# Kernel tuning notes

Measured on AMD Instinct MI355X. Metric: run time of the kernel, lower is better.

The kernel has to match this reference:

```python
import jax, jax.numpy as jnp
import numpy as np

EPS = 1e-3  # Keras BatchNormalization default epsilon
HEADS = 4
KEY_DEPTH = 16   # k
INTRA = 1        # u
VAL_DEPTH = 64   # v = kernel_out // heads = 256 // 4
C_IN = 256
B, HH, WW = 16, 32, 32
N = HH * WW      # == size of positional embedding


def setup_inputs() -> dict:
    key = jax.random.key(0)
    ks = jax.random.split(key, 6)
    x = jax.random.normal(ks[0], (B, HH, WW, C_IN), dtype=jnp.float32)
    # 1x1 conv kernels == dense matrices over the channel dim
    Wq = jax.random.normal(ks[1], (C_IN, KEY_DEPTH * HEADS), dtype=jnp.float32) * 0.05
    Wk = jax.random.normal(ks[2], (C_IN, KEY_DEPTH * INTRA), dtype=jnp.float32) * 0.05
    Wv = jax.random.normal(ks[3], (C_IN, VAL_DEPTH * INTRA), dtype=jnp.float32) * 0.05
    # BatchNorm (inference mode) parameters
    gamma_q = jnp.ones((KEY_DEPTH * HEADS,), jnp.float32)
    beta_q = jnp.zeros((KEY_DEPTH * HEADS,), jnp.float32)
    mean_q = jnp.zeros((KEY_DEPTH * HEADS,), jnp.float32)
    var_q = jnp.ones((KEY_DEPTH * HEADS,), jnp.float32)
    gamma_v = jnp.ones((VAL_DEPTH * INTRA,), jnp.float32)
    beta_v = jnp.zeros((VAL_DEPTH * INTRA,), jnp.float32)
    mean_v = jnp.zeros((VAL_DEPTH * INTRA,), jnp.float32)
    var_v = jnp.ones((VAL_DEPTH * INTRA,), jnp.float32)
    # Positional embedding: [size, size, key_depth, intra_depth], uniform init
    E = jax.random.uniform(ks[4], (N, N, KEY_DEPTH, INTRA), dtype=jnp.float32)
    return {
        'x': x, 'Wq': Wq, 'Wk': Wk, 'Wv': Wv,
        'gamma_q': gamma_q, 'beta_q': beta_q, 'mean_q': mean_q, 'var_q': var_q,
        'gamma_v': gamma_v, 'beta_v': beta_v, 'mean_v': mean_v, 'var_v': var_v,
        'E': E,
    }


def _bn(t, gamma, beta, mean, var):
    return gamma * (t - mean) / jnp.sqrt(var + EPS) + beta


def reference(x, Wq, Wk, Wv, gamma_q, beta_q, mean_q, var_q,
              gamma_v, beta_v, mean_v, var_v, E):
    b, hh, ww, _ = x.shape
    n = hh * ww
    # 1x1 conv projections (context c == x)
    q = jnp.einsum('bhwc,cd->bhwd', x, Wq)           # [b,hh,ww,h*k]
    k = jnp.einsum('bhwc,cd->bhwd', x, Wk)           # [b,hh,ww,u*k]
    v = jnp.einsum('bhwc,cd->bhwd', x, Wv)           # [b,hh,ww,u*v]
    q = _bn(q, gamma_q, beta_q, mean_q, var_q)
    v = _bn(v, gamma_v, beta_v, mean_v, var_v)
    # softmax over the channel axis (faithful to the source code)
    k = jax.nn.softmax(k, axis=-1)
    # rearranges: b hh ww (h k) -> b h k n ; b hh ww (u k) -> b u k n ; b hh ww (u v) -> b u v n
    q = q.reshape(b, n, HEADS, KEY_DEPTH).transpose(0, 2, 3, 1)   # [b,h,k,n]
    k = k.reshape(b, n, INTRA, KEY_DEPTH).transpose(0, 2, 3, 1)   # [b,u,k,n]
    v = v.reshape(b, n, INTRA, VAL_DEPTH).transpose(0, 2, 3, 1)   # [b,u,v,n]
    # content lambda: sum over intra-depth and positions
    lam_c = jnp.einsum('bukn,buvn->bkv', k, v)                    # [b,k,v]
    Yc = jnp.einsum('bhkn,bkv->bhvn', q, lam_c)                   # [b,h,v,n]
    # positional lambdas: E[n,m,k,u] contracted with v[b,u,v,m]
    lam_p = jnp.einsum('nmku,buvm->bnkv', E, v)                   # [b,n,k,v]
    Yp = jnp.einsum('bhkn,bnkv->bhvn', q, lam_p)                  # [b,h,v,n]
    Y = Yc + Yp                                                    # [b,h,v,n]
    # b h v n -> b hh ww (h v)
    out = Y.transpose(0, 3, 1, 2).reshape(b, hh, ww, HEADS * VAL_DEPTH)
    return out
```

## Files before the change

### kernel.cpp

```cpp
#include <hip/hip_runtime.h>
#include <stdint.h>

#define EPS 1e-3f

typedef __bf16 bf16x8 __attribute__((ext_vector_type(8)));
typedef float  f32x4  __attribute__((ext_vector_type(4)));

static __device__ __forceinline__ uint16_t f2bf(float f) {
  union { __bf16 b; uint16_t u; } r; r.b = (__bf16)f; return r.u;
}
static __device__ __forceinline__ uint32_t cvt2(float lo, float hi) {
  union { __bf16 b[2]; uint32_t u; } r;
  r.b[0] = (__bf16)lo; r.b[1] = (__bf16)hi;
  return r.u;
}
static __device__ __forceinline__ void gload_lds16(const void* g, void* l) {
  __builtin_amdgcn_global_load_lds(
      (const __attribute__((address_space(1))) unsigned int*)g,
      (__attribute__((address_space(3))) unsigned int*)l, 16, 0, 0);
}

__global__ __launch_bounds__(256) void wprep(
    const float* __restrict__ Wq, const float* __restrict__ Wk,
    const float* __restrict__ Wv, uint16_t* __restrict__ WtP)
{
  const int col = blockIdx.x, t = threadIdx.x;
  float val = (col < 64) ? Wq[t * 64 + col]
            : (col < 80) ? Wk[t * 16 + (col - 64)]
                         : Wv[t * 64 + (col - 80)];
  WtP[col * 264 + t] = f2bf(val);
}

__global__ __launch_bounds__(256) void proj_mfma(
    const float* __restrict__ x, const uint16_t* __restrict__ WtP,
    const float* __restrict__ gq, const float* __restrict__ bq,
    const float* __restrict__ mq, const float* __restrict__ vq,
    const float* __restrict__ gv, const float* __restrict__ bv,
    const float* __restrict__ mv, const float* __restrict__ vvp,
    float* __restrict__ Qf, uint16_t* __restrict__ VbfT,
    float* __restrict__ part)
{
  __shared__ __align__(16) char smem[111616];
  uint16_t* const xA = (uint16_t*)smem;
  char* const Wt = smem + 33792;

  const int t = threadIdx.x;
  const int wid = t >> 6, lane = t & 63;
  const int bid = blockIdx.x;
  const int b = bid >> 4, mc = bid & 15;
  const int r0 = b * 1024 + mc * 64;

#pragma unroll
  for (int i = 0; i < 19; ++i) {
    int off = (i * 256 + t) * 16;
    gload_lds16((const char*)WtP + off, Wt + off);
  }
  {
    const int row = t >> 2, ks0 = (t & 3) * 64;
    const float* src = x + (size_t)(r0 + row) * 256 + ks0;
    uint16_t* dstp = xA + row * 264 + ks0;
#pragma unroll
    for (int i = 0; i < 8; ++i) {
      float4 d0 = *(const float4*)(src + i * 8);
      float4 d1 = *(const float4*)(src + i * 8 + 4);
      uint4 q;
      q.x = cvt2(d0.x, d0.y); q.y = cvt2(d0.z, d0.w);
      q.z = cvt2(d1.x, d1.y); q.w = cvt2(d1.z, d1.w);
      *(uint4*)(dstp + i * 8) = q;
    }
  }
  __syncthreads();

  f32x4 acc[9];
#pragma unroll
  for (int f = 0; f < 9; ++f) acc[f] = f32x4{0.f, 0.f, 0.f, 0.f};
  const int arow = wid * 16 + (lane & 15);
#pragma unroll
  for (int kst = 0; kst < 8; ++kst) {
    const int sb = kst * 64 + ((lane >> 4) << 4);
    bf16x8 af = *(const bf16x8*)((const char*)xA + arow * 528 + sb);
#pragma unroll
    for (int f = 0; f < 9; ++f) {
      const int crow = f * 16 + (lane & 15);
      bf16x8 bfr = *(const bf16x8*)(Wt + crow * 528 + sb);
      acc[f] = __builtin_amdgcn_mfma_f32_16x16x32_bf16(af, bfr, acc[f], 0, 0, 0);
    }
  }

  const int cl = lane & 15;
  const int rbase = wid * 16 + ((lane >> 4) << 2);

  float qs[4], qb[4], qm[4], vs[4], vb[4], vm[4];
#pragma unroll
  for (int f = 0; f < 4; ++f) {
    const int c = f * 16 + cl;
    qs[f] = gq[c] * rsqrtf(vq[c] + EPS); qb[f] = bq[c]; qm[f] = mq[c];
    vs[f] = gv[c] * rsqrtf(vvp[c] + EPS); vb[f] = bv[c]; vm[f] = mv[c];
  }
#pragma unroll
  for (int f = 0; f < 4; ++f)
#pragma unroll
    for (int r = 0; r < 4; ++r)
      Qf[(size_t)(r0 + rbase + r) * 64 + f * 16 + cl] =
          (acc[f][r] - qm[f]) * qs[f] + qb[f];
  float ex[4];
#pragma unroll
  for (int r = 0; r < 4; ++r) {
    float kv = acc[4][r];
    float mx = kv;
#pragma unroll
    for (int d = 1; d < 16; d <<= 1) mx = fmaxf(mx, __shfl_xor(mx, d, 64));
    float e = __expf(kv - mx);
    float sm = e;
#pragma unroll
    for (int d = 1; d < 16; d <<= 1) sm += __shfl_xor(sm, d, 64);
    ex[r] = e / sm;
  }
  float vv[4][4];
#pragma unroll
  for (int f = 0; f < 4; ++f)
#pragma unroll
    for (int r = 0; r < 4; ++r)
      vv[f][r] = (acc[5 + f][r] - vm[f]) * vs[f] + vb[f];

  __syncthreads();
  float* const vt = (float*)smem;
  float* const ks = (float*)(smem + 64 * 65 * 4);
#pragma unroll
  for (int r = 0; r < 4; ++r) ks[(rbase + r) * 20 + cl] = ex[r];
#pragma unroll
  for (int f = 0; f < 4; ++f)
#pragma unroll
    for (int r = 0; r < 4; ++r) vt[(rbase + r) * 65 + f * 16 + cl] = vv[f][r];
  __syncthreads();

  {
    const int v = t & 63, grp = t >> 6;
#pragma unroll
    for (int h = 0; h < 2; ++h) {
      uint4 q;
      q.x = cvt2(vt[(grp * 16 + h * 8 + 0) * 65 + v], vt[(grp * 16 + h * 8 + 1) * 65 + v]);
      q.y = cvt2(vt[(grp * 16 + h * 8 + 2) * 65 + v], vt[(grp * 16 + h * 8 + 3) * 65 + v]);
      q.z = cvt2(vt[(grp * 16 + h * 8 + 4) * 65 + v], vt[(grp * 16 + h * 8 + 5) * 65 + v]);
      q.w = cvt2(vt[(grp * 16 + h * 8 + 6) * 65 + v], vt[(grp * 16 + h * 8 + 7) * 65 + v]);
      *(uint4*)&VbfT[(size_t)(b * 64 + v) * 1024 + mc * 64 + grp * 16 + h * 8] = q;
    }
  }
  {
    const int kq = t >> 6, v = t & 63;
    float a0 = 0.f, a1 = 0.f, a2 = 0.f, a3 = 0.f;
#pragma unroll 4
    for (int m = 0; m < 64; ++m) {
      float vvx = vt[m * 65 + v];
      a0 = fmaf(ks[m * 20 + kq * 4 + 0], vvx, a0);
      a1 = fmaf(ks[m * 20 + kq * 4 + 1], vvx, a1);
      a2 = fmaf(ks[m * 20 + kq * 4 + 2], vvx, a2);
      a3 = fmaf(ks[m * 20 + kq * 4 + 3], vvx, a3);
    }
    float* dst = part + ((size_t)(b * 16 + mc) << 10) + (kq * 4) * 64 + v;
    dst[0] = a0; dst[64] = a1; dst[128] = a2; dst[192] = a3;
  }
}

__global__ __launch_bounds__(256) void lamc_reduce(const float* __restrict__ part,
                                                   float* __restrict__ Lc)
{
  const int gid = blockIdx.x * 256 + threadIdx.x;
  const int b = gid >> 10, r = gid & 1023;
  const float* p = part + ((size_t)b << 14) + r;
  float s = 0.f;
#pragma unroll
  for (int mc = 0; mc < 16; ++mc) s += p[mc << 10];
  Lc[((size_t)b << 10) + r] = s;
}

__global__ __launch_bounds__(512, 2) void gemm_out(
    const float* __restrict__ E,
    const uint16_t* __restrict__ VbfT,
    const float* __restrict__ Qf,
    const float* __restrict__ Lc,
    float* __restrict__ out)
{
  __shared__ __align__(16) char smem[131072];
  char* const A0 = smem;
  char* const B0 = smem + 32768;
  char* const A1 = smem + 65536;
  char* const B1 = smem + 98304;

  const int t = threadIdx.x;
  const int wid = t >> 6, lane = t & 63;
  const int wm = wid >> 2, wn = wid & 3;
  const int bid = blockIdx.x;
  const int xcd = bid & 7, idx = bid >> 3;
  const int rb = xcd * 8 + (idx >> 2);
  const int cb = idx & 3;
  const int col0 = cb * 256;
  const int n0 = rb * 16;
  const int b0i = cb * 4;

  const int kq = t & 3;
  const int mp = (t >> 2) & 31;
  const int nb = t >> 7;
  const float* Eb = E + ((size_t)n0 << 14);

  int awoff[4][4];
#pragma unroll
  for (int it = 0; it < 4; ++it)
#pragma unroll
    for (int j = 0; j < 4; ++j) {
      int row = (it * 4 + nb) * 16 + kq * 4 + j;
      awoff[it][j] = row * 128 + ((mp * 4) ^ ((row & 7) << 4));
    }

  const uint16_t* bptr[4];
  int bdst[4];
  {
    const uint16_t* Bb = VbfT + ((size_t)col0 << 10);
#pragma unroll
    for (int it = 0; it < 4; ++it) {
      int id = it * 512 + t;
      int row = id >> 3, seg = id & 7;
      bptr[it] = Bb + (row << 10) + ((seg ^ (row & 7)) << 3);
      bdst[it] = id * 16;
    }
  }

  f32x4 acc[8][4];
  {
#pragma unroll
    for (int j = 0; j < 4; ++j) {
      const int col = wn * 64 + j * 16 + (lane & 15);
      const int bb = b0i + (col >> 6), v = col & 63;
      const float* lp = Lc + (size_t)(((bb << 4) + ((lane >> 4) << 2)) << 6) + v;
      f32x4 lc;
#pragma unroll
      for (int r = 0; r < 4; ++r) lc[r] = lp[r << 6];
#pragma unroll
      for (int i = 0; i < 8; ++i) acc[i][j] = lc;
    }
  }

  float4 ra[4], rbx[4];

#pragma unroll
  for (int it = 0; it < 4; ++it) {
    size_t base = ((size_t)(it * 4 + nb) << 14) + ((size_t)(mp * 2) << 4) + (kq << 2);
    ra[it]  = *(const float4*)(Eb + base);
    rbx[it] = *(const float4*)(Eb + base + 16);
  }
#pragma unroll
  for (int it = 0; it < 4; ++it) gload_lds16(bptr[it], B0 + bdst[it]);
#pragma unroll
  for (int it = 0; it < 4; ++it) {
    const float* da = (const float*)&ra[it];
    const float* db = (const float*)&rbx[it];
#pragma unroll
    for (int j = 0; j < 4; ++j)
      *(uint32_t*)(A0 + awoff[it][j]) = cvt2(da[j], db[j]);
  }
  __syncthreads();

#pragma unroll 1
  for (int kt = 0; kt < 16; ++kt) {
    char* Ac = (kt & 1) ? A1 : A0;
    char* Bc = (kt & 1) ? B1 : B0;
    char* An = (kt & 1) ? A0 : A1;
    char* Bn = (kt & 1) ? B0 : B1;
    if (kt < 15) {
      const int m0n = (kt + 1) * 64;
#pragma unroll
      for (int it = 0; it < 4; ++it) {
        size_t base = ((size_t)(it * 4 + nb) << 14) +
                      ((size_t)(m0n + mp * 2) << 4) + (kq << 2);
        ra[it]  = *(const float4*)(Eb + base);
        rbx[it] = *(const float4*)(Eb + base + 16);
      }
#pragma unroll
      for (int it = 0; it < 4; ++it) gload_lds16(bptr[it] + m0n, Bn + bdst[it]);
    }
    __builtin_amdgcn_s_setprio(1);
#pragma unroll
    for (int kk = 0; kk < 2; ++kk) {
      bf16x8 a[8], b[4];
      const int s = kk * 4 + (lane >> 4);
#pragma unroll
      for (int i = 0; i < 8; ++i) {
        int row = wm * 128 + i * 16 + (lane & 15);
        a[i] = *(const bf16x8*)(Ac + row * 128 + ((s ^ (row & 7)) << 4));
      }
#pragma unroll
      for (int j = 0; j < 4; ++j) {
        int row = wn * 64 + j * 16 + (lane & 15);
        b[j] = *(const bf16x8*)(Bc + row * 128 + ((s ^ (row & 7)) << 4));
      }
#pragma unroll
      for (int i = 0; i < 8; ++i)
#pragma unroll
        for (int j = 0; j < 4; ++j)
          acc[i][j] = __builtin_amdgcn_mfma_f32_16x16x32_bf16(a[i], b[j], acc[i][j], 0, 0, 0);
    }
    __builtin_amdgcn_s_setprio(0);
    if (kt < 15) {
#pragma unroll
      for (int it = 0; it < 4; ++it) {
        const float* da = (const float*)&ra[it];
        const float* db = (const float*)&rbx[it];
#pragma unroll
        for (int j = 0; j < 4; ++j)
          *(uint32_t*)(An + awoff[it][j]) = cvt2(da[j], db[j]);
      }
    }
    __syncthreads();
  }

  float* Cs = (float*)smem;
#pragma unroll
  for (int p = 0; p < 4; ++p) {
    if (wm == (p >> 1)) {
#pragma unroll
      for (int il = 0; il < 4; ++il) {
        const int i = ((p & 1) << 2) + il;
#pragma unroll
        for (int j = 0; j < 4; ++j) {
          const int col = wn * 64 + j * 16 + (lane & 15);
#pragma unroll
          for (int r = 0; r < 4; ++r) {
            const int rl = il * 16 + ((lane >> 4) << 2) + r;
            Cs[rl * 258 + col] = acc[i][j][r];
          }
        }
      }
    }
    __syncthreads();
    {
      const int v = t & 63;
#pragma unroll
      for (int c = 0; c < 8; ++c) {
        const int combo = (wid << 3) + c;
        const int n_l = combo >> 4;
        const int b_l = (combo >> 2) & 3;
        const int h = combo & 3;
        const int n = n0 + (p << 2) + n_l;
        const int bb = b0i + b_l;
        const float* qp = Qf + (((size_t)(bb << 10) + n) << 6) + (h << 4);
        float sum = 0.f;
#pragma unroll
        for (int k = 0; k < 16; ++k)
          sum = fmaf(qp[k], Cs[((n_l << 4) + k) * 258 + (b_l << 6) + v], sum);
        out[(((size_t)(bb << 10) + n) << 8) + (h << 6) + v] = sum;
      }
    }
    __syncthreads();
  }
}

extern "C" void kernel_launch(void* const* d_in, const int* in_sizes, int n_in,
                              void* d_out, int out_size, void* d_ws, size_t ws_size,
                              hipStream_t stream) {
  const float* x   = (const float*)d_in[0];
  const float* Wq  = (const float*)d_in[1];
  const float* Wk  = (const float*)d_in[2];
  const float* Wv  = (const float*)d_in[3];
  const float* gq  = (const float*)d_in[4];
  const float* bq  = (const float*)d_in[5];
  const float* mq  = (const float*)d_in[6];
  const float* vq  = (const float*)d_in[7];
  const float* gv  = (const float*)d_in[8];
  const float* bv  = (const float*)d_in[9];
  const float* mv  = (const float*)d_in[10];
  const float* vvp = (const float*)d_in[11];
  const float* E   = (const float*)d_in[12];
  float* out = (float*)d_out;

  char* ws = (char*)d_ws;
  uint16_t* VbfT = (uint16_t*)(ws);
  float*    Qf   = (float*)(ws + (size_t)(2 << 20));
  float*    part = (float*)(ws + (size_t)(6 << 20));
  float*    Lc   = (float*)(ws + (size_t)(7 << 20));
  uint16_t* WtP  = (uint16_t*)(ws + (size_t)(7 << 20) + 65536);

  hipLaunchKernelGGL(wprep, dim3(144), dim3(256), 0, stream, Wq, Wk, Wv, WtP);
  hipLaunchKernelGGL(proj_mfma, dim3(256), dim3(256), 0, stream, x, WtP,
                     gq, bq, mq, vq, gv, bv, mv, vvp, Qf, VbfT, part);
  hipLaunchKernelGGL(lamc_reduce, dim3(64), dim3(256), 0, stream, part, Lc);
  hipLaunchKernelGGL(gemm_out, dim3(256), dim3(512), 0, stream, E, VbfT, Qf, Lc, out);
}
```

Before: 72.02 us.

## Load V operand directly from global, halve LDS to raise occupancy

Drops the LDS double buffer for the B (value) operand in gemm_out. Each wave now reads its bf16 fragments straight from global memory (VbfT) inside the inner loop, which halves shared memory to 64KB. The epilogue is reworked into 8 smaller passes so it fits the reduced LDS. This frees LDS for more resident blocks and removes the B staging traffic, but each wave now does redundant global or L2 reads of B, with exposed latency right before the MFMAs.

```diff
diff --git a/kernel.cpp b/kernel.cpp
--- a/kernel.cpp
+++ b/kernel.cpp
@@ -181,11 +181,9 @@
     const float* __restrict__ Lc,
     float* __restrict__ out)
 {
-  __shared__ __align__(16) char smem[131072];
+  __shared__ __align__(16) char smem[65536];
   char* const A0 = smem;
-  char* const B0 = smem + 32768;
-  char* const A1 = smem + 65536;
-  char* const B1 = smem + 98304;
+  char* const A1 = smem + 32768;
 
   const int t = threadIdx.x;
   const int wid = t >> 6, lane = t & 63;
@@ -212,17 +210,11 @@
       awoff[it][j] = row * 128 + ((mp * 4) ^ ((row & 7) << 4));
     }
 
-  const uint16_t* bptr[4];
-  int bdst[4];
-  {
-    const uint16_t* Bb = VbfT + ((size_t)col0 << 10);
-#pragma unroll
-    for (int it = 0; it < 4; ++it) {
-      int id = it * 512 + t;
-      int row = id >> 3, seg = id & 7;
-      bptr[it] = Bb + (row << 10) + ((seg ^ (row & 7)) << 3);
-      bdst[it] = id * 16;
-    }
+  const uint16_t* bbase[4];
+#pragma unroll
+  for (int j = 0; j < 4; ++j) {
+    const int row = col0 + wn * 64 + j * 16 + (lane & 15);
+    bbase[j] = VbfT + ((size_t)row << 10) + ((lane >> 4) << 3);
   }
 
   f32x4 acc[8][4];
@@ -249,8 +241,6 @@
     rbx[it] = *(const float4*)(Eb + base + 16);
   }
 #pragma unroll
-  for (int it = 0; it < 4; ++it) gload_lds16(bptr[it], B0 + bdst[it]);
-#pragma unroll
   for (int it = 0; it < 4; ++it) {
     const float* da = (const float*)&ra[it];
     const float* db = (const float*)&rbx[it];
@@ -263,9 +253,7 @@
 #pragma unroll 1
   for (int kt = 0; kt < 16; ++kt) {
     char* Ac = (kt & 1) ? A1 : A0;
-    char* Bc = (kt & 1) ? B1 : B0;
     char* An = (kt & 1) ? A0 : A1;
-    char* Bn = (kt & 1) ? B0 : B1;
     if (kt < 15) {
       const int m0n = (kt + 1) * 64;
 #pragma unroll
@@ -275,31 +263,28 @@
         ra[it]  = *(const float4*)(Eb + base);
         rbx[it] = *(const float4*)(Eb + base + 16);
       }
-#pragma unroll
-      for (int it = 0; it < 4; ++it) gload_lds16(bptr[it] + m0n, Bn + bdst[it]);
-    }
-    __builtin_amdgcn_s_setprio(1);
+    }
 #pragma unroll
     for (int kk = 0; kk < 2; ++kk) {
       bf16x8 a[8], b[4];
+      const int moff = kt * 64 + kk * 32;
+#pragma unroll
+      for (int j = 0; j < 4; ++j)
+        b[j] = *(const bf16x8*)(bbase[j] + moff);
       const int s = kk * 4 + (lane >> 4);
 #pragma unroll
       for (int i = 0; i < 8; ++i) {
         int row = wm * 128 + i * 16 + (lane & 15);
         a[i] = *(const bf16x8*)(Ac + row * 128 + ((s ^ (row & 7)) << 4));
       }
-#pragma unroll
-      for (int j = 0; j < 4; ++j) {
-        int row = wn * 64 + j * 16 + (lane & 15);
-        b[j] = *(const bf16x8*)(Bc + row * 128 + ((s ^ (row & 7)) << 4));
-      }
+      __builtin_amdgcn_s_setprio(1);
 #pragma unroll
       for (int i = 0; i < 8; ++i)
 #pragma unroll
         for (int j = 0; j < 4; ++j)
           acc[i][j] = __builtin_amdgcn_mfma_f32_16x16x32_bf16(a[i], b[j], acc[i][j], 0, 0, 0);
-    }
-    __builtin_amdgcn_s_setprio(0);
+      __builtin_amdgcn_s_setprio(0);
+    }
     if (kt < 15) {
 #pragma unroll
       for (int it = 0; it < 4; ++it) {
@@ -315,11 +300,11 @@
 
   float* Cs = (float*)smem;
 #pragma unroll
-  for (int p = 0; p < 4; ++p) {
-    if (wm == (p >> 1)) {
-#pragma unroll
-      for (int il = 0; il < 4; ++il) {
-        const int i = ((p & 1) << 2) + il;
+  for (int p = 0; p < 8; ++p) {
+    if (wm == (p >> 2)) {
+#pragma unroll
+      for (int il = 0; il < 2; ++il) {
+        const int i = ((p & 3) << 1) + il;
 #pragma unroll
         for (int j = 0; j < 4; ++j) {
           const int col = wn * 64 + j * 16 + (lane & 15);
@@ -333,14 +318,14 @@
     }
     __syncthreads();
     {
-      const int v = t & 63;
-#pragma unroll
-      for (int c = 0; c < 8; ++c) {
-        const int combo = (wid << 3) + c;
+      const int v = t & 63, g = t >> 6;
+#pragma unroll
+      for (int c = 0; c < 4; ++c) {
+        const int combo = (g << 2) + c;
         const int n_l = combo >> 4;
         const int b_l = (combo >> 2) & 3;
         const int h = combo & 3;
-        const int n = n0 + (p << 2) + n_l;
+        const int n = n0 + (p << 1) + n_l;
         const int bb = b0i + b_l;
         const float* qp = Qf + (((size_t)(bb << 10) + n) << 6) + (h << 4);
         float sum = 0.f;
```

Measured after the change: 88.56 us. 1.23x slower.
